# Performance work log

Measured on AMD Instinct MI355X. Metric: run time of the kernel, lower is better.

## Reference

```python
import jax, jax.numpy as jnp
import numpy as np


def setup_inputs() -> dict:
    key = jax.random.key(0)
    ks = jax.random.split(key, 8)
    T, A, F, H, N, E = 64, 64, 512, 1024, 512, 4
    s1, s2, s3 = 1.0 / np.sqrt(F), 1.0 / np.sqrt(H), 1.0 / np.sqrt(H)
    return {
        "obs": jax.random.normal(ks[0], (T, A, F), dtype=jnp.float32),
        "W1": jax.random.normal(ks[1], (E, F, H), dtype=jnp.float32) * s1,
        "b1": jnp.zeros((E, H), dtype=jnp.float32),
        "W2": jax.random.normal(ks[2], (E, H, H), dtype=jnp.float32) * s2,
        "b2": jnp.zeros((E, H), dtype=jnp.float32),
        "W3": jax.random.normal(ks[3], (E, H, N), dtype=jnp.float32) * s3,
        "b3": jnp.zeros((E, N), dtype=jnp.float32),
        "agent_type": jax.random.randint(ks[4], (T, A), 0, E, dtype=jnp.int32),
    }


def reference(obs, W1, b1, W2, b2, W3, b3, agent_type):
    # distribute_compute: for each type e, gather obs[mask_e], run expert e's
    # MLP, scatter logits back into a zero-init (T, A, n_action) buffer.
    # Dense-equivalent form: run every expert on all tokens, then select the
    # row belonging to each agent's type (masks partition agents, so the
    # zero-init scatter == one-hot select).
    E = W1.shape[0]
    h = jax.nn.relu(jnp.einsum('taf,efh->etah', obs, W1) + b1[:, None, None, :])
    h = jax.nn.relu(jnp.einsum('etah,ehg->etag', h, W2) + b2[:, None, None, :])
    y = jnp.einsum('etah,ehn->etan', h, W3) + b3[:, None, None, :]  # (E,T,A,N)
    sel = jax.nn.one_hot(agent_type, E, dtype=y.dtype)              # (T,A,E)
    out = jnp.einsum('etan,tae->tan', y, sel)                       # (T,A,N)
    return out
```

## Files before the change

kernel.cpp:

```cpp
#include <hip/hip_runtime.h>
#include <stdint.h>

#define T_DIM 64
#define A_DIM 64
#define F_DIM 512
#define H_DIM 1024
#define N_DIM 512
#define E_DIM 4
#define NTOK 4096
#define NTOK_PAD 4224
#define NSLOT 72

typedef __attribute__((ext_vector_type(8))) short short8;
typedef __attribute__((ext_vector_type(4))) short short4v;
typedef __attribute__((ext_vector_type(4))) float f32x4;

__device__ __forceinline__ unsigned short f2bf(float x) {
  unsigned u = __float_as_uint(x);
  u += 0x7fffu + ((u >> 16) & 1u);
  return (unsigned short)(u >> 16);
}
__device__ __forceinline__ float bf2f(unsigned short h) {
  return __uint_as_float(((unsigned)h) << 16);
}
__device__ __forceinline__ void split_bf(float x, short& hi, short& lo) {
  unsigned short h = f2bf(x);
  hi = (short)h;
  lo = (short)f2bf(x - bf2f(h));
}

__device__ __forceinline__ void gload_lds16(const void* g, void* l) {
  __builtin_amdgcn_global_load_lds(
      (const __attribute__((address_space(1))) unsigned int*)g,
      (__attribute__((address_space(3))) unsigned int*)l, 16, 0, 0);
}

__global__ __launch_bounds__(1024) void k_route(const int* __restrict__ at,
                                                int* __restrict__ pos,
                                                int4* __restrict__ slots) {
  __shared__ int wt[16][4];
  __shared__ int woff[16][4];
  __shared__ int soff[4];
  int tid = threadIdx.x;
  int w = tid >> 6, ln = tid & 63;

  int4 a = ((const int4*)at)[tid];
  int c[4] = {0, 0, 0, 0};
  c[a.x]++; c[a.y]++; c[a.z]++; c[a.w]++;

  int inc[4];
#pragma unroll
  for (int e = 0; e < 4; ++e) inc[e] = c[e];
#pragma unroll
  for (int d = 1; d < 64; d <<= 1) {
#pragma unroll
    for (int e = 0; e < 4; ++e) {
      int u = __shfl_up(inc[e], d, 64);
      if (ln >= d) inc[e] += u;
    }
  }
  if (ln == 63) {
#pragma unroll
    for (int e = 0; e < 4; ++e) wt[w][e] = inc[e];
  }
  __syncthreads();
  if (tid == 0) {
    int tot[4] = {0, 0, 0, 0};
    for (int i = 0; i < 16; ++i)
      for (int e = 0; e < 4; ++e) { woff[i][e] = tot[e]; tot[e] += wt[i][e]; }
    int acc = 0;
    int sbase[4];
    for (int e = 0; e < 4; ++e) { sbase[e] = acc; soff[e] = acc; acc += tot[e]; }
    int si = 0;
    for (int e = 0; e < 4; ++e) {
      int cnt = tot[e];
      for (int m = 0; m * 64 < cnt; ++m) {
        int4 s;
        s.x = sbase[e] + m * 64;
        s.y = (cnt - m * 64) < 64 ? (cnt - m * 64) : 64;
        s.z = e; s.w = 0;
        slots[si++] = s;
      }
    }
    int4 z; z.x = 0; z.y = 0; z.z = 0; z.w = 0;
    while (si < NSLOT) slots[si++] = z;
  }
  __syncthreads();
  int excl[4];
#pragma unroll
  for (int e = 0; e < 4; ++e) excl[e] = soff[e] + woff[w][e] + inc[e] - c[e];
  int es[4] = {a.x, a.y, a.z, a.w};
#pragma unroll
  for (int k = 0; k < 4; ++k) {
    int e = es[k];
    pos[tid * 4 + k] = excl[e];
    excl[e]++;
  }
}

__device__ __forceinline__ void wsplit_tile(const float* __restrict__ W,
                                            short* __restrict__ Th,
                                            short* __restrict__ Tl,
                                            int K, int N, int e, int n0, int k0,
                                            float (*tile)[65]) {
  const float* w = W + (size_t)e * K * N;
  int tr = threadIdx.x >> 4;
  int tc = threadIdx.x & 15;
#pragma unroll
  for (int i = 0; i < 4; ++i) {
    int kk = k0 + i * 16 + tr;
    float4 v = *(const float4*)(w + (size_t)kk * N + n0 + tc * 4);
    tile[i * 16 + tr][tc * 4 + 0] = v.x;
    tile[i * 16 + tr][tc * 4 + 1] = v.y;
    tile[i * 16 + tr][tc * 4 + 2] = v.z;
    tile[i * 16 + tr][tc * 4 + 3] = v.w;
  }
  __syncthreads();
#pragma unroll
  for (int i = 0; i < 4; ++i) {
    int nr = i * 16 + tr;
    size_t ob = ((size_t)e * N + (n0 + nr)) * K + k0 + tc * 4;
    short4v hh, ll;
#pragma unroll
    for (int j = 0; j < 4; ++j) {
      float x = tile[tc * 4 + j][nr];
      short h, l;
      split_bf(x, h, l);
      hh[j] = h; ll[j] = l;
    }
    *(short4v*)&Th[ob] = hh;
    *(short4v*)&Tl[ob] = ll;
  }
}

__global__ __launch_bounds__(256) void k_prep(
    const float* __restrict__ obs, const int* __restrict__ pos, int* __restrict__ idx,
    short* __restrict__ oH, short* __restrict__ oL,
    const float* __restrict__ W1, short* __restrict__ w1h, short* __restrict__ w1l,
    const float* __restrict__ W2, short* __restrict__ w2h, short* __restrict__ w2l,
    const float* __restrict__ W3, short* __restrict__ w3h, short* __restrict__ w3l) {
  __shared__ float tile[64][65];
  int b = blockIdx.x;
  if (b < 1024) {
    int tid = threadIdx.x;
    int t = b * 4 + (tid >> 6);
    int ln = tid & 63;
    int p = pos[t];
    if (ln == 0) idx[p] = t;
    const float* src = obs + (size_t)t * F_DIM;
    int base = ln * 8;
    float4 v0 = *(const float4*)(src + base);
    float4 v1 = *(const float4*)(src + base + 4);
    float xs[8] = {v0.x, v0.y, v0.z, v0.w, v1.x, v1.y, v1.z, v1.w};
    short8 hh, ll;
#pragma unroll
    for (int i = 0; i < 8; ++i) {
      short h, l;
      split_bf(xs[i], h, l);
      hh[i] = h; ll[i] = l;
    }
    *(short8*)&oH[(size_t)p * F_DIM + base] = hh;
    *(short8*)&oL[(size_t)p * F_DIM + base] = ll;
  } else if (b < 1536) {
    int i = b - 1024;
    int e = i >> 7, r = i & 127;
    int n0 = (r >> 3) * 64, k0 = (r & 7) * 64;
    wsplit_tile(W1, w1h, w1l, F_DIM, H_DIM, e, n0, k0, tile);
  } else if (b < 2560) {
    int i = b - 1536;
    int e = i >> 8, r = i & 255;
    int n0 = (r >> 4) * 64, k0 = (r & 15) * 64;
    wsplit_tile(W2, w2h, w2l, H_DIM, H_DIM, e, n0, k0, tile);
  } else {
    int i = b - 2560;
    int e = i >> 7, r = i & 127;
    int n0 = (r >> 4) * 64, k0 = (r & 15) * 64;
    wsplit_tile(W3, w3h, w3l, H_DIM, N_DIM, e, n0, k0, tile);
  }
}

template <int K, int NOUT, bool RELU, bool FINAL>
__launch_bounds__(256, 2)
__global__ void k_gemm(const short* __restrict__ Ah, const short* __restrict__ Al,
                       const short* __restrict__ Bh, const short* __restrict__ Bl,
                       const float* __restrict__ bias,
                       short* __restrict__ Ch, short* __restrict__ Cl,
                       float* __restrict__ outF, const int* __restrict__ idx,
                       const int4* __restrict__ slots) {
  constexpr int NT  = NOUT / 128;
  constexpr int NWG = NSLOT * NT;
  int wg   = (blockIdx.x & 7) * (NWG / 8) + (blockIdx.x >> 3);
  int slot = wg / NT;
  int nt   = wg % NT;
  int4 s = slots[slot];
  int rows = s.y;
  if (rows == 0) return;
  int row0 = s.x, e = s.z, row_end = row0 + rows;
  int ncol0 = nt * 128;

  __shared__ short lds[3][12288];

  int tid = threadIdx.x, wave = tid >> 6, ln = tid & 63;
  const short* bPh = Bh + (size_t)e * NOUT * K;
  const short* bPl = Bl + (size_t)e * NOUT * K;

  const short* srcb[6];
#pragma unroll
  for (int r = 0; r < 6; ++r) {
    int g = r * 256 + tid;
    const short* plane; int wc, rb;
    if (g < 256)       { plane = Ah;  wc = g;        rb = row0;  }
    else if (g < 512)  { plane = Al;  wc = g - 256;  rb = row0;  }
    else if (g < 1024) { plane = bPh; wc = g - 512;  rb = ncol0; }
    else               { plane = bPl; wc = g - 1024; rb = ncol0; }
    int prow = wc >> 2;
    int lch  = (wc & 3) ^ ((wc >> 3) & 3);
    srcb[r] = plane + (size_t)(rb + prow) * K + lch * 8;
  }

  int wbase = (tid & ~63) * 8;

  auto stage = [&](int buf, int ks) {
    int k0 = ks * 32;
#pragma unroll
    for (int r = 0; r < 6; ++r)
      gload_lds16(srcb[r] + k0, (void*)&lds[buf][r * 2048 + wbase]);
  };

  f32x4 acc[2][4] = {};
  int wr = wave >> 1, wcn = wave & 1;
  int tm = ln & 15, kg = ln >> 4;

  int aoff[2], boff[4];
#pragma unroll
  for (int i = 0; i < 2; ++i) {
    int arow = wr * 32 + i * 16 + tm;
    aoff[i] = arow * 32 + (kg ^ ((arow >> 1) & 3)) * 8;
  }
#pragma unroll
  for (int j = 0; j < 4; ++j) {
    int brow = wcn * 64 + j * 16 + tm;
    boff[j] = brow * 32 + (kg ^ ((brow >> 1) & 3)) * 8;
  }

  stage(0, 0);
  stage(1, 1);
  constexpr int NK = K / 32;
  int cb = 0, sb = 2;
  for (int ks = 0; ks < NK; ++ks) {
    if (ks < NK - 1) {
      asm volatile("s_waitcnt vmcnt(6)" ::: "memory");
    } else {
      asm volatile("s_waitcnt vmcnt(0)" ::: "memory");
    }
    __builtin_amdgcn_s_barrier();
    asm volatile("" ::: "memory");

    short8 ah[2], al[2], bh[4], bl[4];
#pragma unroll
    for (int i = 0; i < 2; ++i) {
      ah[i] = *(const short8*)&lds[cb][aoff[i]];
      al[i] = *(const short8*)&lds[cb][2048 + aoff[i]];
    }
#pragma unroll
    for (int j = 0; j < 4; ++j) {
      bh[j] = *(const short8*)&lds[cb][4096 + boff[j]];
      bl[j] = *(const short8*)&lds[cb][8192 + boff[j]];
    }
#pragma unroll
    for (int i = 0; i < 2; ++i)
#pragma unroll
      for (int j = 0; j < 4; ++j) {
        acc[i][j] = __builtin_amdgcn_mfma_f32_16x16x32_bf16(ah[i], bh[j], acc[i][j], 0, 0, 0);
        acc[i][j] = __builtin_amdgcn_mfma_f32_16x16x32_bf16(ah[i], bl[j], acc[i][j], 0, 0, 0);
        acc[i][j] = __builtin_amdgcn_mfma_f32_16x16x32_bf16(al[i], bh[j], acc[i][j], 0, 0, 0);
      }

    asm volatile("" ::: "memory");
    __builtin_amdgcn_s_barrier();
    asm volatile("" ::: "memory");
    if (ks + 2 < NK) stage(sb, ks + 2);
    cb = (cb == 2) ? 0 : cb + 1;
    sb = (sb == 2) ? 0 : sb + 1;
  }

  int lcol = ln & 15;
  int lrow4 = (ln >> 4) * 4;
#pragma unroll
  for (int j = 0; j < 4; ++j) {
    int col = ncol0 + wcn * 64 + j * 16 + lcol;
    float bv = bias[(size_t)e * NOUT + col];
#pragma unroll
    for (int i = 0; i < 2; ++i) {
      int gr0 = row0 + wr * 32 + i * 16 + lrow4;
#pragma unroll
      for (int q = 0; q < 4; ++q) {
        int grow = gr0 + q;
        if (grow < row_end) {
          float x = acc[i][j][q] + bv;
          if (RELU) x = fmaxf(x, 0.0f);
          if (FINAL) {
            int token = idx[grow];
            outF[(size_t)token * NOUT + col] = x;
          } else {
            short h, l;
            split_bf(x, h, l);
            Ch[(size_t)grow * NOUT + col] = h;
            Cl[(size_t)grow * NOUT + col] = l;
          }
        }
      }
    }
  }
}

extern "C" void kernel_launch(void* const* d_in, const int* in_sizes, int n_in,
                              void* d_out, int out_size, void* d_ws, size_t ws_size,
                              hipStream_t stream) {
  (void)in_sizes; (void)n_in; (void)out_size; (void)ws_size;
  const float* obs = (const float*)d_in[0];
  const float* W1  = (const float*)d_in[1];
  const float* b1  = (const float*)d_in[2];
  const float* W2  = (const float*)d_in[3];
  const float* b2  = (const float*)d_in[4];
  const float* W3  = (const float*)d_in[5];
  const float* b3  = (const float*)d_in[6];
  const int*   at  = (const int*)d_in[7];
  float* out = (float*)d_out;

  char* w = (char*)d_ws;
  auto carve = [&](size_t bytes) {
    char* p = w;
    w += (bytes + 255) & ~(size_t)255;
    return p;
  };
  int*  pos   = (int*)carve(NTOK * 4);
  int4* slots = (int4*)carve(NSLOT * 16);
  int*  idx   = (int*)carve(NTOK_PAD * 4);
  short* obsH = (short*)carve((size_t)NTOK_PAD * F_DIM * 2);
  short* obsL = (short*)carve((size_t)NTOK_PAD * F_DIM * 2);
  short* h1H  = (short*)carve((size_t)NTOK_PAD * H_DIM * 2);
  short* h1L  = (short*)carve((size_t)NTOK_PAD * H_DIM * 2);
  short* h2H  = (short*)carve((size_t)NTOK_PAD * H_DIM * 2);
  short* h2L  = (short*)carve((size_t)NTOK_PAD * H_DIM * 2);
  short* w1h  = (short*)carve((size_t)E_DIM * H_DIM * F_DIM * 2);
  short* w1l  = (short*)carve((size_t)E_DIM * H_DIM * F_DIM * 2);
  short* w2h  = (short*)carve((size_t)E_DIM * H_DIM * H_DIM * 2);
  short* w2l  = (short*)carve((size_t)E_DIM * H_DIM * H_DIM * 2);
  short* w3h  = (short*)carve((size_t)E_DIM * N_DIM * H_DIM * 2);
  short* w3l  = (short*)carve((size_t)E_DIM * N_DIM * H_DIM * 2);

  k_route<<<1, 1024, 0, stream>>>(at, pos, slots);
  k_prep<<<3072, 256, 0, stream>>>(obs, pos, idx, obsH, obsL,
                                   W1, w1h, w1l, W2, w2h, w2l, W3, w3h, w3l);

  k_gemm<F_DIM, H_DIM, true, false>
      <<<NSLOT * (H_DIM / 128), 256, 0, stream>>>(
          obsH, obsL, w1h, w1l, b1, h1H, h1L, nullptr, nullptr, slots);
  k_gemm<H_DIM, H_DIM, true, false>
      <<<NSLOT * (H_DIM / 128), 256, 0, stream>>>(
          h1H, h1L, w2h, w2l, b2, h2H, h2L, nullptr, nullptr, slots);
  k_gemm<H_DIM, N_DIM, false, true>
      <<<NSLOT * (N_DIM / 128), 256, 0, stream>>>(
          h2H, h2L, w3h, w3l, b3, nullptr, nullptr, out, idx, slots);
}
```

Measured before the change: 219.7 us.

## Store operands in pre-tiled K-chunk layout and use double-buffered LDS pipeline

Activations and split weights are now written in a blocked layout (64-row by 32-k tiles for A, 128-col by 32-k tiles for B), so each GEMM stage loads one contiguous chunk instead of strided rows. Each expert's row range is padded to a multiple of 64 so A tiles align with slots, which enlarges the padded token buffer. The GEMM drops from a triple-buffered vmcnt-based pipeline to a double-buffered one with full __syncthreads, which frees LDS so occupancy can rise to 3 blocks per SIMD group. The catch is less prefetch depth and heavier synchronization in exchange for contiguous loads and higher occupancy.

```diff
diff --git a/kernel.cpp b/kernel.cpp
--- a/kernel.cpp
+++ b/kernel.cpp
@@ -8,7 +8,7 @@
 #define N_DIM 512
 #define E_DIM 4
 #define NTOK 4096
-#define NTOK_PAD 4224
+#define NTOK_PAD 4352
 #define NSLOT 72
 
 typedef __attribute__((ext_vector_type(8))) short short8;
@@ -70,7 +70,10 @@
       for (int e = 0; e < 4; ++e) { woff[i][e] = tot[e]; tot[e] += wt[i][e]; }
     int acc = 0;
     int sbase[4];
-    for (int e = 0; e < 4; ++e) { sbase[e] = acc; soff[e] = acc; acc += tot[e]; }
+    for (int e = 0; e < 4; ++e) {
+      sbase[e] = acc; soff[e] = acc;
+      acc += (tot[e] + 63) & ~63;
+    }
     int si = 0;
     for (int e = 0; e < 4; ++e) {
       int cnt = tot[e];
@@ -101,9 +104,10 @@
 __device__ __forceinline__ void wsplit_tile(const float* __restrict__ W,
                                             short* __restrict__ Th,
                                             short* __restrict__ Tl,
-                                            int K, int N, int e, int n0, int k0,
-                                            float (*tile)[65]) {
+                                            int K, int N, int NB, int e, int n0,
+                                            int k0, float (*tile)[65]) {
   const float* w = W + (size_t)e * K * N;
+  int KT = K >> 5;
   int tr = threadIdx.x >> 4;
   int tc = threadIdx.x & 15;
 #pragma unroll
@@ -119,7 +123,9 @@
 #pragma unroll
   for (int i = 0; i < 4; ++i) {
     int nr = i * 16 + tr;
-    size_t ob = ((size_t)e * N + (n0 + nr)) * K + k0 + tc * 4;
+    int n = n0 + nr;
+    int k = k0 + tc * 4;
+    size_t ob = ((((size_t)e * NB + (n >> 7)) * KT + (k >> 5)) * 128 + (n & 127)) * 32 + (k & 31);
     short4v hh, ll;
 #pragma unroll
     for (int j = 0; j < 4; ++j) {
@@ -159,28 +165,30 @@
       split_bf(xs[i], h, l);
       hh[i] = h; ll[i] = l;
     }
-    *(short8*)&oH[(size_t)p * F_DIM + base] = hh;
-    *(short8*)&oL[(size_t)p * F_DIM + base] = ll;
+    size_t tb = ((size_t)(p >> 6) * (F_DIM / 32) + (base >> 5)) * 2048 +
+                (size_t)(p & 63) * 32 + (base & 31);
+    *(short8*)&oH[tb] = hh;
+    *(short8*)&oL[tb] = ll;
   } else if (b < 1536) {
     int i = b - 1024;
     int e = i >> 7, r = i & 127;
     int n0 = (r >> 3) * 64, k0 = (r & 7) * 64;
-    wsplit_tile(W1, w1h, w1l, F_DIM, H_DIM, e, n0, k0, tile);
+    wsplit_tile(W1, w1h, w1l, F_DIM, H_DIM, H_DIM / 128, e, n0, k0, tile);
   } else if (b < 2560) {
     int i = b - 1536;
     int e = i >> 8, r = i & 255;
     int n0 = (r >> 4) * 64, k0 = (r & 15) * 64;
-    wsplit_tile(W2, w2h, w2l, H_DIM, H_DIM, e, n0, k0, tile);
+    wsplit_tile(W2, w2h, w2l, H_DIM, H_DIM, H_DIM / 128, e, n0, k0, tile);
   } else {
     int i = b - 2560;
     int e = i >> 7, r = i & 127;
     int n0 = (r >> 4) * 64, k0 = (r & 15) * 64;
-    wsplit_tile(W3, w3h, w3l, H_DIM, N_DIM, e, n0, k0, tile);
+    wsplit_tile(W3, w3h, w3l, H_DIM, N_DIM, N_DIM / 128, e, n0, k0, tile);
   }
 }
 
 template <int K, int NOUT, bool RELU, bool FINAL>
-__launch_bounds__(256, 2)
+__launch_bounds__(256, 3)
 __global__ void k_gemm(const short* __restrict__ Ah, const short* __restrict__ Al,
                        const short* __restrict__ Bh, const short* __restrict__ Bl,
                        const float* __restrict__ bias,
@@ -188,6 +196,8 @@
                        float* __restrict__ outF, const int* __restrict__ idx,
                        const int4* __restrict__ slots) {
   constexpr int NT  = NOUT / 128;
+  constexpr int KT  = K / 32;
+  constexpr int KTN = NOUT / 32;
   constexpr int NWG = NSLOT * NT;
   int wg   = (blockIdx.x & 7) * (NWG / 8) + (blockIdx.x >> 3);
   int slot = wg / NT;
@@ -198,33 +208,28 @@
   int row0 = s.x, e = s.z, row_end = row0 + rows;
   int ncol0 = nt * 128;
 
-  __shared__ short lds[3][12288];
+  __shared__ short lds[2][12288];
 
   int tid = threadIdx.x, wave = tid >> 6, ln = tid & 63;
-  const short* bPh = Bh + (size_t)e * NOUT * K;
-  const short* bPl = Bl + (size_t)e * NOUT * K;
-
+
+  size_t abase = (size_t)(row0 >> 6) * KT * 2048;
+  size_t bbase = ((size_t)e * NT + nt) * KT * 4096;
+  auto swz = [](int c) { return (c >> 2) * 32 + ((c & 3) ^ ((c >> 3) & 3)) * 8; };
   const short* srcb[6];
-#pragma unroll
-  for (int r = 0; r < 6; ++r) {
-    int g = r * 256 + tid;
-    const short* plane; int wc, rb;
-    if (g < 256)       { plane = Ah;  wc = g;        rb = row0;  }
-    else if (g < 512)  { plane = Al;  wc = g - 256;  rb = row0;  }
-    else if (g < 1024) { plane = bPh; wc = g - 512;  rb = ncol0; }
-    else               { plane = bPl; wc = g - 1024; rb = ncol0; }
-    int prow = wc >> 2;
-    int lch  = (wc & 3) ^ ((wc >> 3) & 3);
-    srcb[r] = plane + (size_t)(rb + prow) * K + lch * 8;
-  }
+  srcb[0] = Ah + abase + swz(tid);
+  srcb[1] = Al + abase + swz(tid);
+  srcb[2] = Bh + bbase + swz(tid);
+  srcb[3] = Bh + bbase + swz(tid + 256);
+  srcb[4] = Bl + bbase + swz(tid);
+  srcb[5] = Bl + bbase + swz(tid + 256);
+  const int STR[6] = {2048, 2048, 4096, 4096, 4096, 4096};
 
   int wbase = (tid & ~63) * 8;
 
-  auto stage = [&](int buf, int ks) {
-    int k0 = ks * 32;
+  auto stage = [&](int buf, int kt) {
 #pragma unroll
     for (int r = 0; r < 6; ++r)
-      gload_lds16(srcb[r] + k0, (void*)&lds[buf][r * 2048 + wbase]);
+      gload_lds16(srcb[r] + (size_t)STR[r] * kt, (void*)&lds[buf][r * 2048 + wbase]);
   };
 
   f32x4 acc[2][4] = {};
@@ -244,18 +249,10 @@
   }
 
   stage(0, 0);
-  stage(1, 1);
-  constexpr int NK = K / 32;
-  int cb = 0, sb = 2;
-  for (int ks = 0; ks < NK; ++ks) {
-    if (ks < NK - 1) {
-      asm volatile("s_waitcnt vmcnt(6)" ::: "memory");
-    } else {
-      asm volatile("s_waitcnt vmcnt(0)" ::: "memory");
-    }
-    __builtin_amdgcn_s_barrier();
-    asm volatile("" ::: "memory");
-
+  __syncthreads();
+  for (int ks = 0; ks < KT; ++ks) {
+    int cb = ks & 1;
+    if (ks + 1 < KT) stage(cb ^ 1, ks + 1);
     short8 ah[2], al[2], bh[4], bl[4];
 #pragma unroll
     for (int i = 0; i < 2; ++i) {
@@ -275,13 +272,7 @@
         acc[i][j] = __builtin_amdgcn_mfma_f32_16x16x32_bf16(ah[i], bl[j], acc[i][j], 0, 0, 0);
         acc[i][j] = __builtin_amdgcn_mfma_f32_16x16x32_bf16(al[i], bh[j], acc[i][j], 0, 0, 0);
       }
-
-    asm volatile("" ::: "memory");
-    __builtin_amdgcn_s_barrier();
-    asm volatile("" ::: "memory");
-    if (ks + 2 < NK) stage(sb, ks + 2);
-    cb = (cb == 2) ? 0 : cb + 1;
-    sb = (sb == 2) ? 0 : sb + 1;
+    __syncthreads();
   }
 
   int lcol = ln & 15;
@@ -305,8 +296,10 @@
           } else {
             short h, l;
             split_bf(x, h, l);
-            Ch[(size_t)grow * NOUT + col] = h;
-            Cl[(size_t)grow * NOUT + col] = l;
+            size_t hb = ((size_t)(grow >> 6) * KTN + (col >> 5)) * 2048 +
+                        (size_t)(grow & 63) * 32 + (col & 31);
+            Ch[hb] = h;
+            Cl[hb] = l;
           }
         }
       }
```

New measurement: 192.9 us. -12.2%, faster.
